# Kernel tuning notes

Measured on AMD Instinct MI355X. Metric: run time of the kernel, lower is better.

The kernel has to match this reference:

```python
import jax, jax.numpy as jnp
import numpy as np

N_SEGMENT = 8
N_DIV = 8
C = 256            # net.in_channels
O = 256            # net.out_channels (1x1 conv)
NT, H, W = 128, 28, 28


def _make_shift_weights():
    """Replicates MsCEGroupConv1d.weight_init(); returns per-channel temporal
    kernels as [channels, k] float32 arrays (cross-correlation taps)."""
    planes = C // 4
    fold = planes // N_DIV
    w3 = np.zeros((C // 2, 3), np.float32)
    w3[:2 * fold, 0] = 1.0
    w3[2 * fold:4 * fold, 2] = 1.0
    w3[4 * fold:, 1] = 1.0
    w5 = np.zeros((planes, 5), np.float32)
    w5[:fold, :2] = 1.0
    w5[fold:2 * fold, 3:] = 1.0
    w5[2 * fold:, 2] = 1.0
    w7 = np.zeros((planes, 7), np.float32)
    w7[:fold, :3] = 1.0
    w7[fold:2 * fold, 4:] = 1.0
    w7[2 * fold:, 3] = 1.0
    return jnp.asarray(w3), jnp.asarray(w5), jnp.asarray(w7)


def setup_inputs() -> dict:
    key = jax.random.key(0)
    k1, k2, k3 = jax.random.split(key, 3)
    x = jax.random.normal(k1, (NT, C, H, W), dtype=jnp.float32)
    w3, w5, w7 = _make_shift_weights()
    # wrapped net: 1x1 Conv2d(C -> O) with bias (PyTorch default init scale)
    bound = 1.0 / np.sqrt(C)
    net_w = jax.random.uniform(k2, (O, C), jnp.float32, -bound, bound)
    net_b = jax.random.uniform(k3, (O,), jnp.float32, -bound, bound)
    return {"x": x, "w3": w3, "w5": w5, "w7": w7, "net_w": net_w, "net_b": net_b}


def _dwconv_t(x, w):
    """Depthwise temporal conv. x: [nb, c, T, h, w], w: [c, k], 'same' padding.
    Matches torch Conv3d(kernel=(k,1,1), padding=(k//2,0,0), groups=c)."""
    k = w.shape[1]
    p = k // 2
    T = x.shape[2]
    xp = jnp.pad(x, ((0, 0), (0, 0), (p, p), (0, 0), (0, 0)))
    out = w[None, :, 0, None, None, None] * jax.lax.dynamic_slice_in_dim(xp, 0, T, axis=2)
    for i in range(1, k):
        out = out + w[None, :, i, None, None, None] * jax.lax.dynamic_slice_in_dim(xp, i, T, axis=2)
    return out


def reference(x, w3, w5, w7, net_w, net_b):
    nt, c, h, w = x.shape
    nb = nt // N_SEGMENT
    # [nt,c,h,w] -> [nb, c, T, h, w]
    xt = x.reshape(nb, N_SEGMENT, c, h, w).transpose(0, 2, 1, 3, 4)
    x3 = xt[:, : c // 2]
    x5 = xt[:, c // 2 : c // 2 + c // 4]
    x7 = xt[:, c // 2 + c // 4 :]
    y3 = _dwconv_t(x3, w3)
    y5 = _dwconv_t(x5, w5)
    y7 = _dwconv_t(x7, w7)
    y = jnp.concatenate([y3, y5, y7], axis=1)        # [nb, c, T, h, w]
    y = y.transpose(0, 2, 1, 3, 4).reshape(nt, c, h, w)
    # net: 1x1 Conv2d
    out = jnp.einsum('nchw,oc->nohw', y, net_w) + net_b[None, :, None, None]
    return out
```

## Files before the change

kernel.cpp:

```cpp
#include <hip/hip_runtime.h>
#include <hip/hip_bf16.h>

typedef __attribute__((ext_vector_type(8))) short short8;
typedef __attribute__((ext_vector_type(4))) float f32x4;
typedef __attribute__((ext_vector_type(4))) unsigned int u32x4;

#define C_TOT 256
#define O_TOT 256
#define HW_   784
#define NT_   128
#define KMAX  1792
#define KPAD_STD 352
#define XBYTES (NT_ * C_TOT * HW_ * 4)
#define MARKER 0x60000000u

#define WS_IDX_OFF  16
#define WS_CVAL_OFF (WS_IDX_OFF + 4 * KMAX)
#define WS_OFFT_OFF (WS_CVAL_OFF + 4 * KMAX)
#define WS_A3_OFF   (WS_OFFT_OFF + 4 * 8 * KMAX)

#if __has_builtin(__builtin_amdgcn_make_buffer_rsrc) && __has_builtin(__builtin_amdgcn_raw_buffer_load_b32)
#define USE_RAW_BUF 1
#else
#define USE_RAW_BUF 0
#endif

__device__ __forceinline__ unsigned int pk2(float lo, float hi) {
    float2 f; f.x = lo; f.y = hi;
    __hip_bfloat162 h = __float22bfloat162_rn(f);
    unsigned int r;
    __builtin_memcpy(&r, &h, 4);
    return r;
}
__device__ __forceinline__ unsigned short f2b(float f) {
    union { float f; unsigned int u; } cv; cv.f = f;
    unsigned int u = cv.u;
    u += 0x7fffu + ((u >> 16) & 1u);
    return (unsigned short)(u >> 16);
}

__global__ __launch_bounds__(256)
void build_idx(const float* __restrict__ w3, const float* __restrict__ w5,
               const float* __restrict__ w7, unsigned int* __restrict__ meta,
               unsigned int* __restrict__ idx, float* __restrict__ cval,
               unsigned int* __restrict__ offt)
{
    const int c = threadIdx.x;
    float cf[7];
    #pragma unroll
    for (int i = 0; i < 7; ++i) cf[i] = 0.f;
    if (c < 128) {
        #pragma unroll
        for (int i = 0; i < 3; ++i) cf[i + 2] = w3[c * 3 + i];
    } else if (c < 192) {
        #pragma unroll
        for (int i = 0; i < 5; ++i) cf[i + 1] = w5[(c - 128) * 5 + i];
    } else {
        #pragma unroll
        for (int i = 0; i < 7; ++i) cf[i] = w7[(c - 192) * 7 + i];
    }
    int cnt = 0;
    #pragma unroll
    for (int i = 0; i < 7; ++i) cnt += (cf[i] != 0.f);

    __shared__ int sc[256];
    sc[c] = cnt;
    __syncthreads();
    for (int off = 1; off < 256; off <<= 1) {
        int u = 0;
        if (c >= off) u = sc[c - off];
        __syncthreads();
        sc[c] += u;
        __syncthreads();
    }
    const int start = sc[c] - cnt;
    int J = sc[255];
    if (J > KMAX) J = KMAX;
    int Kpad = (J + 31) & ~31;
    if (Kpad > KMAX) Kpad = KMAX;
    if (c == 0) { meta[0] = (unsigned int)Kpad; meta[1] = (unsigned int)J; }

    int j = start;
    #pragma unroll
    for (int i = 0; i < 7; ++i) {
        if (cf[i] != 0.f) {
            if (j < KMAX) {
                idx[j] = (unsigned int)c | ((unsigned int)i << 8);
                cval[j] = cf[i];
                const int dt  = i - 3;
                const int lin = (dt * C_TOT + c) * (HW_ * 4);
                #pragma unroll
                for (int tt = 0; tt < 8; ++tt) {
                    const int tf = tt + dt;
                    offt[tt * KMAX + j] =
                        (tf >= 0 && tf < 8) ? (unsigned int)lin : MARKER;
                }
            }
            ++j;
        }
    }
    for (int p = J + c; p < Kpad; p += 256) {
        idx[p] = 3u << 8;
        cval[p] = 0.f;
        #pragma unroll
        for (int tt = 0; tt < 8; ++tt) offt[tt * KMAX + p] = MARKER;
    }
}

__global__ __launch_bounds__(256)
void build_A3(const float* __restrict__ netw, const unsigned int* __restrict__ meta,
              const unsigned int* __restrict__ idx, const float* __restrict__ cval,
              unsigned short* __restrict__ A3)
{
    const int o = blockIdx.x;
    const int Kpad   = (int)meta[0];
    const int nslots = Kpad >> 3;
    for (int s = threadIdx.x; s < nslots; s += 256) {
        unsigned short v[8];
        #pragma unroll
        for (int e = 0; e < 8; ++e) {
            const int jj = s * 8 + e;
            const int c  = (int)(idx[jj] & 255u);
            v[e] = f2b(netw[o * C_TOT + c] * cval[jj]);
        }
        *reinterpret_cast<u32x4*>(&A3[((size_t)s * 256 + o) * 8]) =
            *reinterpret_cast<const u32x4*>(v);
    }
}

__global__ __launch_bounds__(256, 3)
void msce_gather(const float* __restrict__ x,
                 const unsigned short* __restrict__ A3,
                 const unsigned int* __restrict__ offt,
                 const unsigned int* __restrict__ meta,
                 const float* __restrict__ net_b,
                 float* __restrict__ out)
{
    const int Kpad = (int)meta[0];
    const int KK   = Kpad >> 5;

    const int tid  = threadIdx.x;
    const int wave = tid >> 6;
    const int lane = tid & 63;

#if USE_RAW_BUF
    const __amdgpu_buffer_rsrc_t rsrc =
        __builtin_amdgcn_make_buffer_rsrc((void*)x, (short)0,
                                          (int)XBYTES, 0x00020000);
    #define GLOAD(ofs) __builtin_bit_cast(float, \
        __builtin_amdgcn_raw_buffer_load_b32(rsrc, (int)(ofs), 0, 0))
#else
    #define GLOAD(ofs) (((ofs) < (unsigned int)XBYTES) ? x[(ofs) >> 2] : 0.f)
#endif

    const int bid  = blockIdx.x;
    const int work = (bid & 7) * 208 + (bid >> 3);
    const int n    = work / 13;
    const int tile = work - n * 13;
    const int p0   = (tile < 12) ? tile * 64 : 720;
    const int t    = n & 7;

    const int og   = wave;
    const int koct = lane >> 4;
    const int prow = lane & 15;
    const unsigned int n_off = (unsigned int)n * (unsigned int)(C_TOT * HW_ * 4);
    const unsigned int* offrow = offt + (size_t)t * KMAX;

    f32x4 acc[4][4];
    #pragma unroll
    for (int ms = 0; ms < 4; ++ms) {
        const f32x4 b = *reinterpret_cast<const f32x4*>(
                            &net_b[og * 64 + ms * 16 + koct * 4]);
        #pragma unroll
        for (int ns = 0; ns < 4; ++ns) acc[ms][ns] = b;
    }

    auto step = [&](int kk) {
        unsigned int off8[8];
        #pragma unroll
        for (int e = 0; e < 8; ++e)
            off8[e] = offrow[kk * 32 + koct * 8 + e];

        short8 af[4];
        const unsigned short* abase =
            A3 + ((size_t)(kk * 4 + koct) * 256 + og * 64 + prow) * 8;
        #pragma unroll
        for (int ms = 0; ms < 4; ++ms)
            af[ms] = *reinterpret_cast<const short8*>(abase + (size_t)ms * 16 * 8);

        short8 bfr[4];
        #pragma unroll
        for (int ns = 0; ns < 4; ++ns) {
            const unsigned int pofs = n_off + (unsigned int)((p0 + ns * 16 + prow) * 4);
            float g[8];
            #pragma unroll
            for (int e = 0; e < 8; ++e)
                g[e] = GLOAD(off8[e] + pofs);
            u32x4 bw;
            bw[0] = pk2(g[0], g[1]);
            bw[1] = pk2(g[2], g[3]);
            bw[2] = pk2(g[4], g[5]);
            bw[3] = pk2(g[6], g[7]);
            bfr[ns] = __builtin_bit_cast(short8, bw);
        }

        #pragma unroll
        for (int ms = 0; ms < 4; ++ms)
            #pragma unroll
            for (int ns = 0; ns < 4; ++ns)
                acc[ms][ns] = __builtin_amdgcn_mfma_f32_16x16x32_bf16(
                                  af[ms], bfr[ns], acc[ms][ns], 0, 0, 0);
    };

    if (Kpad == KPAD_STD) {
        #pragma unroll
        for (int kk = 0; kk < 11; ++kk) step(kk);
    } else {
        for (int kk = 0; kk < KK; ++kk) step(kk);
    }
    #undef GLOAD

    #pragma unroll
    for (int ns = 0; ns < 4; ++ns) {
        const int p = p0 + ns * 16 + prow;
        #pragma unroll
        for (int ms = 0; ms < 4; ++ms) {
            const int o = og * 64 + ms * 16 + koct * 4;
            const size_t base = ((size_t)n * O_TOT + o) * HW_ + p;
            #pragma unroll
            for (int r = 0; r < 4; ++r)
                out[base + (size_t)r * HW_] = acc[ms][ns][r];
        }
    }
}

extern "C" void kernel_launch(void* const* d_in, const int* in_sizes, int n_in,
                              void* d_out, int out_size, void* d_ws, size_t ws_size,
                              hipStream_t stream) {
    const float* x    = (const float*)d_in[0];
    const float* w3p  = (const float*)d_in[1];
    const float* w5p  = (const float*)d_in[2];
    const float* w7p  = (const float*)d_in[3];
    const float* netw = (const float*)d_in[4];
    const float* netb = (const float*)d_in[5];
    float* outp = (float*)d_out;

    char* ws = (char*)d_ws;
    unsigned int*   meta = (unsigned int*)ws;
    unsigned int*   idx  = (unsigned int*)(ws + WS_IDX_OFF);
    float*          cval = (float*)(ws + WS_CVAL_OFF);
    unsigned int*   offt = (unsigned int*)(ws + WS_OFFT_OFF);
    unsigned short* A3   = (unsigned short*)(ws + WS_A3_OFF);

    hipLaunchKernelGGL(build_idx, dim3(1), dim3(256), 0, stream,
                       w3p, w5p, w7p, meta, idx, cval, offt);
    hipLaunchKernelGGL(build_A3, dim3(256), dim3(256), 0, stream,
                       netw, meta, idx, cval, A3);

    hipLaunchKernelGGL(msce_gather, dim3(1664), dim3(256), 0, stream,
                       x, A3, offt, meta, netb, outp);
}
```

Before: 61.79 us.

## Software-pipeline gather loads one K-step ahead of MFMA compute

The fixed-K path now double-buffers offsets, A fragments and gathered x values, issuing step k+1's buffer loads before computing step k. The goal is to hide global gather latency behind MFMA work inside a wave. Keeping two sets of 32 gathered floats plus A fragments raises register pressure, so launch bounds drop from 3 to 2 blocks per SIMD-unit target, which lowers occupancy. Pixel offsets are also hoisted out of the loop.

```diff
diff --git a/kernel.cpp b/kernel.cpp
--- a/kernel.cpp
+++ b/kernel.cpp
@@ -128,7 +128,7 @@
     }
 }
 
-__global__ __launch_bounds__(256, 3)
+__global__ __launch_bounds__(256, 2)
 void msce_gather(const float* __restrict__ x,
                  const unsigned short* __restrict__ A3,
                  const unsigned int* __restrict__ offt,
@@ -166,6 +166,11 @@
     const unsigned int n_off = (unsigned int)n * (unsigned int)(C_TOT * HW_ * 4);
     const unsigned int* offrow = offt + (size_t)t * KMAX;
 
+    unsigned int pofs[4];
+    #pragma unroll
+    for (int ns = 0; ns < 4; ++ns)
+        pofs[ns] = n_off + (unsigned int)((p0 + ns * 16 + prow) * 4);
+
     f32x4 acc[4][4];
     #pragma unroll
     for (int ms = 0; ms < 4; ++ms) {
@@ -175,35 +180,36 @@
         for (int ns = 0; ns < 4; ++ns) acc[ms][ns] = b;
     }
 
-    auto step = [&](int kk) {
-        unsigned int off8[8];
+    auto load_off = [&](int kk, unsigned int (&o8)[8]) {
         #pragma unroll
         for (int e = 0; e < 8; ++e)
-            off8[e] = offrow[kk * 32 + koct * 8 + e];
-
-        short8 af[4];
+            o8[e] = offrow[kk * 32 + koct * 8 + e];
+    };
+    auto load_af = [&](int kk, short8 (&af)[4]) {
         const unsigned short* abase =
             A3 + ((size_t)(kk * 4 + koct) * 256 + og * 64 + prow) * 8;
         #pragma unroll
         for (int ms = 0; ms < 4; ++ms)
             af[ms] = *reinterpret_cast<const short8*>(abase + (size_t)ms * 16 * 8);
-
-        short8 bfr[4];
-        #pragma unroll
-        for (int ns = 0; ns < 4; ++ns) {
-            const unsigned int pofs = n_off + (unsigned int)((p0 + ns * 16 + prow) * 4);
-            float g[8];
+    };
+    auto issue_g = [&](const unsigned int (&o8)[8], float (&g)[32]) {
+        #pragma unroll
+        for (int ns = 0; ns < 4; ++ns)
             #pragma unroll
             for (int e = 0; e < 8; ++e)
-                g[e] = GLOAD(off8[e] + pofs);
+                g[ns * 8 + e] = GLOAD(o8[e] + pofs[ns]);
+    };
+    auto compute = [&](const short8 (&af)[4], const float (&g)[32]) {
+        short8 bfr[4];
+        #pragma unroll
+        for (int ns = 0; ns < 4; ++ns) {
             u32x4 bw;
-            bw[0] = pk2(g[0], g[1]);
-            bw[1] = pk2(g[2], g[3]);
-            bw[2] = pk2(g[4], g[5]);
-            bw[3] = pk2(g[6], g[7]);
+            bw[0] = pk2(g[ns * 8 + 0], g[ns * 8 + 1]);
+            bw[1] = pk2(g[ns * 8 + 2], g[ns * 8 + 3]);
+            bw[2] = pk2(g[ns * 8 + 4], g[ns * 8 + 5]);
+            bw[3] = pk2(g[ns * 8 + 6], g[ns * 8 + 7]);
             bfr[ns] = __builtin_bit_cast(short8, bw);
         }
-
         #pragma unroll
         for (int ms = 0; ms < 4; ++ms)
             #pragma unroll
@@ -213,10 +219,36 @@
     };
 
     if (Kpad == KPAD_STD) {
-        #pragma unroll
-        for (int kk = 0; kk < 11; ++kk) step(kk);
+        unsigned int o8_[2][8];
+        short8       af_[2][4];
+        float        g_[2][32];
+
+        load_off(0, o8_[0]);
+        load_off(1, o8_[1]);
+        load_af(0, af_[0]);
+        issue_g(o8_[0], g_[0]);
+
+        #pragma unroll
+        for (int kk = 0; kk < 11; ++kk) {
+            const int cur = kk & 1, nxt = (kk + 1) & 1;
+            if (kk + 1 < 11) {
+                load_af(kk + 1, af_[nxt]);
+                issue_g(o8_[nxt], g_[nxt]);
+            }
+            if (kk + 2 < 11)
+                load_off(kk + 2, o8_[cur]);
+            compute(af_[cur], g_[cur]);
+        }
     } else {
-        for (int kk = 0; kk < KK; ++kk) step(kk);
+        for (int kk = 0; kk < KK; ++kk) {
+            unsigned int o8[8];
+            short8 af[4];
+            float g[32];
+            load_off(kk, o8);
+            load_af(kk, af);
+            issue_g(o8, g);
+            compute(af, g);
+        }
     }
     #undef GLOAD
 
```

New measurement: 61.07 us. About the same (-1.2%).
